# Kernel optimization log

Measured on AMD Instinct MI355X. Metric: run time of the kernel, lower is better.

## Reference

```python
import jax, jax.numpy as jnp
import numpy as np

B, H, N = 512, 128, 32      # batch, horizon, lidar sectors
D = 75                      # state dim (32 sectors + 32 diff + 11 non-lidar)
NON_AUG = 17                # 11 non-lidar + 6 aux stats
SM = 32                     # sector_model_dim
HALF = 128                  # embed_dim // 2
EMB = 256                   # embed_dim
DYAW_IDX = 72               # 64 + 3 + 2 + 2 + 1
NO_ECHO = 0.95


def linear(x, W, b):
    # torch nn.Linear: y = x @ W.T + b, W: (out, in)
    return jnp.einsum('...i,oi->...o', x, W) + b


def layernorm(x, w, b, eps=1e-5):
    m = x.mean(-1, keepdims=True)
    v = ((x - m) ** 2).mean(-1, keepdims=True)
    return (x - m) / jnp.sqrt(v + eps) * w + b


def setup_inputs() -> dict:
    key = jax.random.key(0)
    ks = jax.random.split(key, 10)
    f32 = jnp.float32
    return {
        'state_seq': jax.random.uniform(ks[0], (B, H, D), dtype=f32),
        'token_W': jax.random.normal(ks[1], (SM, 3), dtype=f32) * 0.3,
        'token_b': jnp.zeros((SM,), f32),
        'query_W': jax.random.normal(ks[2], (SM, NON_AUG), dtype=f32) * 0.2,
        'query_b': jnp.zeros((SM,), f32),
        'range_bias_scale': jnp.asarray(1.0, f32),
        'valid_bias': jnp.asarray(0.0, f32),
        'invalid_bias': jnp.asarray(-1.0, f32),
        'att_ln_w': jnp.ones((SM,), f32),
        'att_ln_b': jnp.zeros((SM,), f32),
        'non_W': jax.random.normal(ks[3], (HALF, NON_AUG), dtype=f32) * 0.2,
        'non_b': jnp.zeros((HALF,), f32),
        'spfb_W': jax.random.normal(ks[4], (HALF, 3), dtype=f32) * 0.3,
        'spfb_b': jnp.zeros((HALF,), f32),
        'sp_gate': jnp.asarray(-4.0, f32),
        'spatial_W': jax.random.normal(ks[5], (HALF, SM), dtype=f32) * 0.15,
        'spatial_b': jnp.zeros((HALF,), f32),
        'fuse_W': jax.random.normal(ks[6], (EMB, 2 * HALF), dtype=f32) * 0.06,
        'fuse_b': jnp.zeros((EMB,), f32),
        'ln_w': jnp.ones((EMB,), f32),
        'ln_b': jnp.zeros((EMB,), f32),
    }


def _forward(state_seq, token_W, token_b, query_W, query_b,
             range_bias_scale, valid_bias, invalid_bias, att_ln_w, att_ln_b,
             non_W, non_b, spfb_W, spfb_b, sp_gate,
             spatial_W, spatial_b, fuse_W, fuse_b, ln_w, ln_b):
    sectors = state_seq[:, :, 0:N]            # (B,H,N)
    lidar_diff = state_seq[:, :, N:2 * N]     # (B,H,N)
    non_lidar = state_seq[:, :, 2 * N:D]      # (B,H,11)

    valid = (sectors < NO_ECHO).astype(state_seq.dtype)
    min_r = sectors.min(axis=-1)
    mean_r = sectors.mean(axis=-1)
    valid_ratio = valid.mean(axis=-1)
    diff_abs = jnp.abs(lidar_diff)
    diff_abs_mean = diff_abs.mean(axis=-1)
    diff_abs_max = diff_abs.max(axis=-1)
    dyaw_abs = jnp.clip(jnp.abs(state_seq[:, :, DYAW_IDX]), 0.0, 1.0)
    diff_mag = jnp.clip(diff_abs_mean, 0.0, 1.0)

    aux = jnp.stack([min_r, mean_r, valid_ratio, diff_abs_mean, diff_abs_max, dyaw_abs], axis=-1)
    non_aug = jnp.concatenate([non_lidar, aux], axis=-1)  # (B,H,17)
    non_emb = jax.nn.relu(linear(non_aug, non_W, non_b))  # (B,H,HALF)

    sp_fallback = jnp.stack([min_r, mean_r, valid_ratio], axis=-1)
    sp_fallback_emb = jax.nn.relu(linear(sp_fallback, spfb_W, spfb_b))

    # --- spatial sector attention ---
    tok = jnp.stack([sectors, lidar_diff, valid], axis=-1)        # (B,H,N,3)
    tok_emb = jax.nn.relu(linear(tok, token_W, token_b))          # (B,H,N,SM)
    q = jax.nn.relu(linear(non_aug, query_W, query_b))[:, :, None, :]  # (B,H,1,SM)
    score = (tok_emb * q).sum(axis=-1) / np.sqrt(SM)              # (B,H,N)
    score = score + range_bias_scale * (1.0 - sectors)
    score = score + valid_bias * valid + invalid_bias * (1.0 - valid)
    w = jax.nn.softmax(score, axis=-1)
    ctx = (w[..., None] * tok_emb).sum(axis=2)                    # (B,H,SM)
    ctx = layernorm(ctx, att_ln_w, att_ln_b)

    sp_att_emb = jax.nn.relu(linear(ctx, spatial_W, spatial_b))
    alpha = jax.nn.sigmoid(sp_gate)
    sp_emb = alpha * sp_att_emb + (1.0 - alpha) * sp_fallback_emb

    x = jnp.concatenate([non_emb, sp_emb], axis=-1)
    x = jax.nn.relu(linear(x, fuse_W, fuse_b))
    x = layernorm(x, ln_w, ln_b)
    time_feats = jnp.stack([diff_mag, dyaw_abs], axis=-1)
    return x, time_feats


def reference(state_seq, token_W, token_b, query_W, query_b,
              range_bias_scale, valid_bias, invalid_bias, att_ln_w, att_ln_b,
              non_W, non_b, spfb_W, spfb_b, sp_gate,
              spatial_W, spatial_b, fuse_W, fuse_b, ln_w, ln_b):
    return _forward(state_seq, token_W, token_b, query_W, query_b,
                    range_bias_scale, valid_bias, invalid_bias, att_ln_w, att_ln_b,
                    non_W, non_b, spfb_W, spfb_b, sp_gate,
                    spatial_W, spatial_b, fuse_W, fuse_b, ln_w, ln_b)
```

## Files before the change

### kernel.cpp

```cpp
#include <hip/hip_runtime.h>

#define BH      65536
#define DSTATE  75
#define EMBD    256
#define NROWS   16
#define NTHREADS 512
#define NBLOCKS (BH / NROWS)

typedef _Float16 h2    __attribute__((ext_vector_type(2)));
typedef _Float16 f16x8 __attribute__((ext_vector_type(8)));
typedef float    f32x4 __attribute__((ext_vector_type(4)));

__device__ __forceinline__ h2 u2h(unsigned int u) {
    union { unsigned int u; h2 h; } c; c.u = u; return c.h;
}
__device__ __forceinline__ unsigned int h2u(h2 h) {
    union { h2 h; unsigned int u; } c; c.h = h; return c.u;
}
__device__ __forceinline__ unsigned int packh2(float a, float b) {
    union { h2 h; unsigned int u; } c;
    c.h = h2{(_Float16)a, (_Float16)b}; return c.u;
}
__device__ __forceinline__ h2 pkrtz(float a, float b) {
#if __has_builtin(__builtin_amdgcn_cvt_pkrtz)
    auto r = __builtin_amdgcn_cvt_pkrtz(a, b);
    return *reinterpret_cast<h2*>(&r);
#else
    return h2{(_Float16)a, (_Float16)b};
#endif
}
__device__ __forceinline__ float fdot2(h2 a, h2 b, float c) {
#if __has_builtin(__builtin_amdgcn_fdot2)
    return __builtin_amdgcn_fdot2(a, b, c, false);
#else
    return c + (float)a[0] * (float)b[0] + (float)a[1] * (float)b[1];
#endif
}
__device__ __forceinline__ h2 pkfma(h2 a, h2 b, h2 c) {
#if __has_builtin(__builtin_elementwise_fma)
    return __builtin_elementwise_fma(a, b, c);
#else
    return a * b + c;
#endif
}

template<int CTRL>
__device__ __forceinline__ float dppmv(float x) {
    return __builtin_bit_cast(float,
        __builtin_amdgcn_update_dpp(0, __builtin_bit_cast(int, x), CTRL, 0xF, 0xF, true));
}
template<int IMM>
__device__ __forceinline__ float swz(float x) {
    return __builtin_bit_cast(float,
        __builtin_amdgcn_ds_swizzle(__builtin_bit_cast(int, x), IMM));
}
#define ROR1 0x121
#define ROR2 0x122
#define ROR4 0x124
#define ROR8 0x128
#define QXOR1 0xB1
#define SWZ_XOR16 0x401F
#define SWZ_BC8   0x0100

__device__ __forceinline__ float sum32(float x) {
    x += dppmv<ROR1>(x); x += dppmv<ROR2>(x);
    x += dppmv<ROR4>(x); x += dppmv<ROR8>(x);
    return x + swz<SWZ_XOR16>(x);
}
__device__ __forceinline__ float sum16(float x) {
    x += dppmv<ROR1>(x); x += dppmv<ROR2>(x);
    x += dppmv<ROR4>(x); x += dppmv<ROR8>(x);
    return x;
}

__global__ __launch_bounds__(256) void prep_w_kernel(
    const float* __restrict__ fuse_W, const float* __restrict__ non_W,
    const float* __restrict__ spatial_W, const float* __restrict__ query_W,
    const float* __restrict__ token_W, const float* __restrict__ token_b,
    unsigned short* __restrict__ ws)
{
    int id = blockIdx.x * 256 + threadIdx.x;
    if (id < 8192) {
        int wl = id & 63, ct = (id >> 6) & 15, ks = id >> 10;
        int n = ct * 16 + (wl & 15);
        int k0 = ks * 32 + (wl >> 4) * 8;
        const float* src = fuse_W + n * 256 + k0;
        float4 a = *reinterpret_cast<const float4*>(src);
        float4 b = *reinterpret_cast<const float4*>(src + 4);
        uint4 o = make_uint4(packh2(a.x, a.y), packh2(a.z, a.w),
                             packh2(b.x, b.y), packh2(b.z, b.w));
        reinterpret_cast<uint4*>(ws)[id] = o;
    } else if (id < 8704) {
        int i = id - 8192;
        int wl = i & 63, ct = i >> 6;
        int n = ct * 16 + (wl & 15);
        int k0 = (wl >> 4) * 8;
        float v[8];
        #pragma unroll
        for (int j = 0; j < 8; ++j) {
            int k = k0 + j;
            v[j] = (k < 17) ? non_W[n * 17 + k] : 0.0f;
        }
        uint4 o = make_uint4(packh2(v[0], v[1]), packh2(v[2], v[3]),
                             packh2(v[4], v[5]), packh2(v[6], v[7]));
        reinterpret_cast<uint4*>(ws)[8192 + i] = o;
    } else if (id < 9216) {
        int i = id - 8704;
        int wl = i & 63, ct = i >> 6;
        int n = ct * 16 + (wl & 15);
        int k0 = (wl >> 4) * 8;
        const float* src = spatial_W + n * 32 + k0;
        float4 a = *reinterpret_cast<const float4*>(src);
        float4 b = *reinterpret_cast<const float4*>(src + 4);
        uint4 o = make_uint4(packh2(a.x, a.y), packh2(a.z, a.w),
                             packh2(b.x, b.y), packh2(b.z, b.w));
        reinterpret_cast<uint4*>(ws)[8704 + i] = o;
    } else if (id < 9728) {
        int i = id - 9216;
        int feat = i >> 4, j = i & 15;
        int k0 = 2 * j, k1 = 2 * j + 1;
        float a = (k0 < 17) ? query_W[feat * 17 + k0] : 0.0f;
        float b = (k1 < 17) ? query_W[feat * 17 + k1] : 0.0f;
        unsigned int* qWh = reinterpret_cast<unsigned int*>(ws + 73728);
        qWh[i] = packh2(a, b);
    } else if (id < 9856) {
        int i = id - 9728;
        int tbl = i >> 5, k = i & 31;
        float v = (tbl < 3) ? token_W[3 * k + tbl] : token_b[k];
        unsigned int* TWb = reinterpret_cast<unsigned int*>(ws + 73728) + 512;
        TWb[i] = packh2(v, v);
    } else if (id < 9920) {
        int i = id - 9856;
        int tbl = i >> 4, j = i & 15;
        int k0 = 2 * j, k1 = 2 * j + 1;
        float a = (tbl < 3) ? token_W[3 * k0 + tbl] : token_b[k0];
        float b = (tbl < 3) ? token_W[3 * k1 + tbl] : token_b[k1];
        unsigned int* TWp = reinterpret_cast<unsigned int*>(ws + 73728) + 640;
        TWp[i] = packh2(a, b);
    }
}

__global__ __launch_bounds__(512, 4) void att_state_enc_kernel(
    const float* __restrict__ state,
    const float* __restrict__ query_b,
    const float* __restrict__ rbs_p, const float* __restrict__ vb_p, const float* __restrict__ ivb_p,
    const float* __restrict__ att_ln_w, const float* __restrict__ att_ln_b,
    const float* __restrict__ non_b,
    const float* __restrict__ spfb_W, const float* __restrict__ spfb_b,
    const float* __restrict__ sp_gate_p,
    const float* __restrict__ spatial_b,
    const unsigned short* __restrict__ Wf, const unsigned short* __restrict__ Wn,
    const unsigned short* __restrict__ Ws,
    const unsigned int* __restrict__ qWh, const unsigned int* __restrict__ TWb,
    const unsigned int* __restrict__ TWp,
    const float* __restrict__ fuse_b,
    const float* __restrict__ ln_w, const float* __restrict__ ln_b,
    float* __restrict__ out_x, float* __restrict__ out_tf)
{
    __shared__ __align__(16) float4 s_fb4[NROWS];
    __shared__ __align__(16) _Float16 s_na_h[NROWS][40];
    __shared__ __align__(16) _Float16 s_ctx_h[NROWS][40];
    __shared__ __align__(16) unsigned int s_q2[NROWS][16];
    __shared__ __align__(16) uint4 s_p4[NROWS][16];
    __shared__ __align__(16) _Float16 s_x[NROWS][280];
    __shared__ __align__(16) float2 s_part[NROWS][8];
    __shared__ __align__(16) float2 s_mr[NROWS];
    __shared__ float  s_tf[NROWS * 2];

    const int t = threadIdx.x;
    const int g = t >> 5;
    const int l = t & 31;
    const long rowbase = (long)blockIdx.x * NROWS;

    const float rbs = rbs_p[0];
    const float vb  = vb_p[0];
    const float ivb = ivb_p[0];

    const float qb = query_b[l];
    const uint4* qwp = reinterpret_cast<const uint4*>(qWh + l * 16);
    const uint4 qw0 = qwp[0], qw1 = qwp[1], qw2 = qwp[2];
    const h2 zero2 = h2{(_Float16)0.0f, (_Float16)0.0f};

    {
        const int row = g;
        const long gb = (rowbase + row) * DSTATE;

        float sec = state[gb + l];
        float dif = state[gb + 32 + l];
        float nl  = (l < 11) ? state[gb + 64 + l] : 0.0f;
        float vld = (sec < 0.95f) ? 1.0f : 0.0f;
        float da  = fabsf(dif);
        float mn = sec, sm = sec, vs = vld, ds = da, dmx = da;
        {
            mn = fminf(mn, dppmv<ROR1>(mn)); sm += dppmv<ROR1>(sm); vs += dppmv<ROR1>(vs);
            ds += dppmv<ROR1>(ds); dmx = fmaxf(dmx, dppmv<ROR1>(dmx));
            mn = fminf(mn, dppmv<ROR2>(mn)); sm += dppmv<ROR2>(sm); vs += dppmv<ROR2>(vs);
            ds += dppmv<ROR2>(ds); dmx = fmaxf(dmx, dppmv<ROR2>(dmx));
            mn = fminf(mn, dppmv<ROR4>(mn)); sm += dppmv<ROR4>(sm); vs += dppmv<ROR4>(vs);
            ds += dppmv<ROR4>(ds); dmx = fmaxf(dmx, dppmv<ROR4>(dmx));
            mn = fminf(mn, dppmv<ROR8>(mn)); sm += dppmv<ROR8>(sm); vs += dppmv<ROR8>(vs);
            ds += dppmv<ROR8>(ds); dmx = fmaxf(dmx, dppmv<ROR8>(dmx));
            mn = fminf(mn, swz<SWZ_XOR16>(mn)); sm += swz<SWZ_XOR16>(sm);
            vs += swz<SWZ_XOR16>(vs); ds += swz<SWZ_XOR16>(ds);
            dmx = fmaxf(dmx, swz<SWZ_XOR16>(dmx));
        }
        const float min_r = mn, mean_r = sm * (1.0f/32.0f), vr = vs * (1.0f/32.0f);
        const float dam = ds * (1.0f/32.0f), dax = dmx;
        const float dyaw = fminf(fabsf(swz<SWZ_BC8>(nl)), 1.0f);

        float naval = 0.0f;
        if (l < 11)       naval = nl;
        else if (l == 11) naval = min_r;
        else if (l == 12) naval = mean_r;
        else if (l == 13) naval = vr;
        else if (l == 14) naval = dam;
        else if (l == 15) naval = dax;
        else if (l == 16) naval = dyaw;
        s_na_h[row][l] = (_Float16)naval;
        if (l == 0) {
            s_fb4[row] = make_float4(min_r, mean_r, vr, 0.0f);
            s_tf[row * 2] = fminf(dam, 1.0f); s_tf[row * 2 + 1] = dyaw;
        }

        {
            const uint4* nap = reinterpret_cast<const uint4*>(&s_na_h[row][0]);
            uint4 n0 = nap[0], n1 = nap[1], n2 = nap[2];
            float a0 = qb, a1 = 0.0f;
            a0 = fdot2(u2h(qw0.x), u2h(n0.x), a0);
            a1 = fdot2(u2h(qw0.y), u2h(n0.y), a1);
            a0 = fdot2(u2h(qw0.z), u2h(n0.z), a0);
            a1 = fdot2(u2h(qw0.w), u2h(n0.w), a1);
            a0 = fdot2(u2h(qw1.x), u2h(n1.x), a0);
            a1 = fdot2(u2h(qw1.y), u2h(n1.y), a1);
            a0 = fdot2(u2h(qw1.z), u2h(n1.z), a0);
            a1 = fdot2(u2h(qw1.w), u2h(n1.w), a1);
            a0 = fdot2(u2h(qw2.x), u2h(n2.x), a0);
            float qv = fmaxf(a0 + a1, 0.0f);
            float qn = dppmv<QXOR1>(qv);
            if ((l & 1) == 0) s_q2[row][l >> 1] = h2u(pkrtz(qv, qn));
        }

        {
            unsigned int q2[16];
            *reinterpret_cast<uint4*>(&q2[0])  = *reinterpret_cast<const uint4*>(&s_q2[row][0]);
            *reinterpret_cast<uint4*>(&q2[4])  = *reinterpret_cast<const uint4*>(&s_q2[row][4]);
            *reinterpret_cast<uint4*>(&q2[8])  = *reinterpret_cast<const uint4*>(&s_q2[row][8]);
            *reinterpret_cast<uint4*>(&q2[12]) = *reinterpret_cast<const uint4*>(&s_q2[row][12]);
            const h2 sec2 = pkrtz(sec, sec);
            const h2 dif2 = pkrtz(dif, dif);
            const h2 vld2 = pkrtz(vld, vld);
            float a0 = 0.0f, a1 = 0.0f;
            #pragma unroll
            for (int j = 0; j < 16; j += 2) {
                h2 z0 = pkfma(vld2, u2h(TWp[32 + j]), u2h(TWp[48 + j]));
                z0 = pkfma(dif2, u2h(TWp[16 + j]), z0);
                z0 = pkfma(sec2, u2h(TWp[j]), z0);
                z0 = __builtin_elementwise_max(z0, zero2);
                a0 = fdot2(z0, u2h(q2[j]), a0);
                h2 z1 = pkfma(vld2, u2h(TWp[33 + j]), u2h(TWp[49 + j]));
                z1 = pkfma(dif2, u2h(TWp[17 + j]), z1);
                z1 = pkfma(sec2, u2h(TWp[1 + j]), z1);
                z1 = __builtin_elementwise_max(z1, zero2);
                a1 = fdot2(z1, u2h(q2[j + 1]), a1);
            }
            float score = (a0 + a1) * 0.17677669529663687f
                        + rbs * (1.0f - sec) + vb * vld + ivb * (1.0f - vld);
            score = fminf(fmaxf(score, -60.0f), 60.0f);
            float e = __expf(score - 20.0f);
            float se = sum32(e);
            float w = __fdividef(e, se);
            float wn = dppmv<QXOR1>(w);
            float sn = dppmv<QXOR1>(sec);
            float dn = dppmv<QXOR1>(dif);
            float vn = dppmv<QXOR1>(vld);
            if ((l & 1) == 0) {
                uint4 pk = make_uint4(h2u(pkrtz(w, wn)), h2u(pkrtz(sec, sn)),
                                      h2u(pkrtz(dif, dn)), h2u(pkrtz(vld, vn)));
                s_p4[row][l >> 1] = pk;
            }
        }

        {
            const h2 tw0b = u2h(TWb[l]);
            const h2 tw1b = u2h(TWb[32 + l]);
            const h2 tw2b = u2h(TWb[64 + l]);
            const h2 tbb  = u2h(TWb[96 + l]);
            float a0 = 0.0f, a1 = 0.0f;
            #pragma unroll
            for (int i = 0; i < 16; i += 2) {
                uint4 p0 = s_p4[row][i];
                h2 z0 = pkfma(u2h(p0.w), tw2b, tbb);
                z0 = pkfma(u2h(p0.z), tw1b, z0);
                z0 = pkfma(u2h(p0.y), tw0b, z0);
                z0 = __builtin_elementwise_max(z0, zero2);
                a0 = fdot2(u2h(p0.x), z0, a0);
                uint4 p1 = s_p4[row][i + 1];
                h2 z1 = pkfma(u2h(p1.w), tw2b, tbb);
                z1 = pkfma(u2h(p1.z), tw1b, z1);
                z1 = pkfma(u2h(p1.y), tw0b, z1);
                z1 = __builtin_elementwise_max(z1, zero2);
                a1 = fdot2(u2h(p1.x), z1, a1);
            }
            float acc = a0 + a1;
            float smv = acc, sq = acc * acc;
            smv += dppmv<ROR1>(smv); sq += dppmv<ROR1>(sq);
            smv += dppmv<ROR2>(smv); sq += dppmv<ROR2>(sq);
            smv += dppmv<ROR4>(smv); sq += dppmv<ROR4>(sq);
            smv += dppmv<ROR8>(smv); sq += dppmv<ROR8>(sq);
            smv += swz<SWZ_XOR16>(smv); sq += swz<SWZ_XOR16>(sq);
            float mean = smv * (1.0f/32.0f);
            float var  = sq * (1.0f/32.0f) - mean * mean;
            float rstd = rsqrtf(var + 1e-5f);
            float ctx = (acc - mean) * rstd * att_ln_w[l] + att_ln_b[l];
            s_ctx_h[row][l] = (_Float16)ctx;
        }
    }
    __syncthreads();

    const int wid = t >> 6, wl = t & 63;
    const int arow = wl & 15, kg = wl >> 4;

    {
        if (t < NROWS * 2) out_tf[rowbase * 2 + t] = s_tf[t];

        const float alpha = 1.0f / (1.0f + __expf(-sp_gate_p[0]));
        float mnr[4], mer[4], vrr[4];
        #pragma unroll
        for (int r = 0; r < 4; ++r) {
            float4 fb4 = s_fb4[kg * 4 + r];
            mnr[r] = fb4.x; mer[r] = fb4.y; vrr[r] = fb4.z;
        }
        f16x8 a_na  = *reinterpret_cast<const f16x8*>(&s_na_h[arow][kg * 8]);
        f16x8 a_ctx = *reinterpret_cast<const f16x8*>(&s_ctx_h[arow][kg * 8]);

        const int ct = wid;
        const int col = ct * 16 + arow;
        f16x8 bN = *reinterpret_cast<const f16x8*>(Wn + ((ct * 64) + wl) * 8);
        f16x8 bS = *reinterpret_cast<const f16x8*>(Ws + ((ct * 64) + wl) * 8);
        f32x4 accN = __builtin_amdgcn_mfma_f32_16x16x32_f16(a_na,  bN, f32x4{0.f,0.f,0.f,0.f}, 0,0,0);
        f32x4 accS = __builtin_amdgcn_mfma_f32_16x16x32_f16(a_ctx, bS, f32x4{0.f,0.f,0.f,0.f}, 0,0,0);
        const float nb = non_b[col], sb = spatial_b[col];
        const float w0 = spfb_W[col*3], w1 = spfb_W[col*3+1], w2 = spfb_W[col*3+2];
        const float fbb = spfb_b[col];
        #pragma unroll
        for (int r = 0; r < 4; ++r) {
            const int row = kg * 4 + r;
            float ne = fmaxf(accN[r] + nb, 0.0f);
            float sa = fmaxf(accS[r] + sb, 0.0f);
            float fb = fmaxf(fbb + w0*mnr[r] + w1*mer[r] + w2*vrr[r], 0.0f);
            float sp = alpha * sa + (1.0f - alpha) * fb;
            float nen = dppmv<QXOR1>(ne);
            float spn = dppmv<QXOR1>(sp);
            if ((arow & 1) == 0) {
                *reinterpret_cast<unsigned int*>(&s_x[row][col])       = h2u(pkrtz(ne, nen));
                *reinterpret_cast<unsigned int*>(&s_x[row][128 + col]) = h2u(pkrtz(sp, spn));
            }
        }
    }
    __syncthreads();

    float v[2][4];
    {
        f32x4 acc[2];
        #pragma unroll
        for (int i = 0; i < 2; ++i) acc[i] = f32x4{0.f, 0.f, 0.f, 0.f};
        #pragma unroll
        for (int ks = 0; ks < 8; ++ks) {
            f16x8 a = *reinterpret_cast<const f16x8*>(&s_x[arow][ks * 32 + kg * 8]);
            #pragma unroll
            for (int i = 0; i < 2; ++i) {
                const int ct = wid * 2 + i;
                f16x8 b = *reinterpret_cast<const f16x8*>(Wf + (((ks * 16 + ct) * 64) + wl) * 8);
                acc[i] = __builtin_amdgcn_mfma_f32_16x16x32_f16(a, b, acc[i], 0, 0, 0);
            }
        }
        float psum[4] = {0.f, 0.f, 0.f, 0.f};
        float psq[4]  = {0.f, 0.f, 0.f, 0.f};
        #pragma unroll
        for (int i = 0; i < 2; ++i) {
            const int col = (wid * 2 + i) * 16 + arow;
            const float bias = fuse_b[col];
            #pragma unroll
            for (int r = 0; r < 4; ++r) {
                float x = fmaxf(acc[i][r] + bias, 0.0f);
                v[i][r] = x;
                psum[r] += x;
                psq[r]  += x * x;
            }
        }
        #pragma unroll
        for (int r = 0; r < 4; ++r) {
            psum[r] = sum16(psum[r]);
            psq[r]  = sum16(psq[r]);
        }
        if (arow == 0) {
            #pragma unroll
            for (int r = 0; r < 4; ++r)
                s_part[kg * 4 + r][wid] = make_float2(psum[r], psq[r]);
        }
    }
    __syncthreads();

    if (t < NROWS) {
        const float4* pp = reinterpret_cast<const float4*>(&s_part[t][0]);
        float4 pa = pp[0], pb = pp[1], pc = pp[2], pd = pp[3];
        float sum = pa.x + pa.z + pb.x + pb.z + pc.x + pc.z + pd.x + pd.z;
        float sq  = pa.y + pa.w + pb.y + pb.w + pc.y + pc.w + pd.y + pd.w;
        float mean = sum * (1.0f/256.0f);
        float var  = sq * (1.0f/256.0f) - mean * mean;
        float rstd = rsqrtf(var + 1e-5f);
        s_mr[t] = make_float2(mean, rstd);
    }
    __syncthreads();

    {
        float lwv[2], lbv[2];
        #pragma unroll
        for (int i = 0; i < 2; ++i) {
            const int col = (wid * 2 + i) * 16 + arow;
            lwv[i] = ln_w[col]; lbv[i] = ln_b[col];
        }
        #pragma unroll
        for (int r = 0; r < 4; ++r) {
            const int row = kg * 4 + r;
            float2 mr = s_mr[row];
            const long obase = (rowbase + row) * EMBD;
            #pragma unroll
            for (int i = 0; i < 2; ++i) {
                const int col = (wid * 2 + i) * 16 + arow;
                out_x[obase + col] = (v[i][r] - mr.x) * mr.y * lwv[i] + lbv[i];
            }
        }
    }
}

extern "C" void kernel_launch(void* const* d_in, const int* in_sizes, int n_in,
                              void* d_out, int out_size, void* d_ws, size_t ws_size,
                              hipStream_t stream) {
    const float* state     = (const float*)d_in[0];
    const float* token_W   = (const float*)d_in[1];
    const float* token_b   = (const float*)d_in[2];
    const float* query_W   = (const float*)d_in[3];
    const float* query_b   = (const float*)d_in[4];
    const float* rbs       = (const float*)d_in[5];
    const float* vbias     = (const float*)d_in[6];
    const float* ivbias    = (const float*)d_in[7];
    const float* att_ln_w  = (const float*)d_in[8];
    const float* att_ln_b  = (const float*)d_in[9];
    const float* non_W     = (const float*)d_in[10];
    const float* non_b     = (const float*)d_in[11];
    const float* spfb_W    = (const float*)d_in[12];
    const float* spfb_b    = (const float*)d_in[13];
    const float* sp_gate   = (const float*)d_in[14];
    const float* spatial_W = (const float*)d_in[15];
    const float* spatial_b = (const float*)d_in[16];
    const float* fuse_W    = (const float*)d_in[17];
    const float* fuse_b    = (const float*)d_in[18];
    const float* ln_w      = (const float*)d_in[19];
    const float* ln_b      = (const float*)d_in[20];

    float* out_x  = (float*)d_out;
    float* out_tf = out_x + (size_t)BH * EMBD;

    unsigned short* wsu = (unsigned short*)d_ws;
    const unsigned short* Wf = wsu;
    const unsigned short* Wn = wsu + 65536;
    const unsigned short* Ws = wsu + 65536 + 4096;
    const unsigned int* qWh = (const unsigned int*)(wsu + 73728);
    const unsigned int* TWb = qWh + 512;
    const unsigned int* TWp = TWb + 128;

    hipLaunchKernelGGL(prep_w_kernel, dim3(39), dim3(256), 0, stream,
                       fuse_W, non_W, spatial_W, query_W, token_W, token_b, wsu);

    hipLaunchKernelGGL(att_state_enc_kernel, dim3(NBLOCKS), dim3(NTHREADS), 0, stream,
        state, query_b, rbs, vbias, ivbias,
        att_ln_w, att_ln_b, non_b, spfb_W, spfb_b, sp_gate, spatial_b,
        Wf, Wn, Ws, qWh, TWb, TWp, fuse_b, ln_w, ln_b, out_x, out_tf);
}
```

Before: 57.00 us.

## Split fused encoder into front attention kernel and back MFMA kernel via workspace

Splits the single fused kernel into two. A front kernel handles the per-row stats, query, softmax attention and context layernorm with 8 rows per 256-thread block, and writes fp16 packed non-aug/ctx vectors plus fallback stats to workspace. A back kernel then does the MFMA projections, fuse GEMM and final layernorm on 32 rows per block, so each fuse-weight fetch is reused across more rows. The aim is to stop the two phases from limiting each other's occupancy and to improve weight reuse, at the cost of an extra launch and an intermediate global round-trip. The fused path stays as a fallback when the workspace is too small.

```diff
diff --git a/kernel.cpp b/kernel.cpp
--- a/kernel.cpp
+++ b/kernel.cpp
@@ -3,9 +3,6 @@
 #define BH      65536
 #define DSTATE  75
 #define EMBD    256
-#define NROWS   16
-#define NTHREADS 512
-#define NBLOCKS (BH / NROWS)
 
 typedef _Float16 h2    __attribute__((ext_vector_type(2)));
 typedef _Float16 f16x8 __attribute__((ext_vector_type(8)));
@@ -140,6 +137,312 @@
     }
 }
 
+__global__ __launch_bounds__(256, 8) void front_kernel(
+    const float* __restrict__ state,
+    const float* __restrict__ query_b,
+    const float* __restrict__ rbs_p, const float* __restrict__ vb_p, const float* __restrict__ ivb_p,
+    const float* __restrict__ att_ln_w, const float* __restrict__ att_ln_b,
+    const unsigned int* __restrict__ qWh, const unsigned int* __restrict__ TWb,
+    const unsigned int* __restrict__ TWp,
+    unsigned int* __restrict__ g_na, unsigned int* __restrict__ g_ctx,
+    float4* __restrict__ g_fb, float* __restrict__ out_tf)
+{
+    __shared__ __align__(16) _Float16 s_na_h[8][40];
+    __shared__ __align__(16) unsigned int s_q2[8][16];
+    __shared__ __align__(16) uint4 s_p4[8][16];
+
+    const int t = threadIdx.x;
+    const int g = t >> 5;
+    const int l = t & 31;
+    const long row = (long)blockIdx.x * 8 + g;
+    const long gb = row * DSTATE;
+
+    const float rbs = rbs_p[0];
+    const float vb  = vb_p[0];
+    const float ivb = ivb_p[0];
+    const float qb = query_b[l];
+    const uint4* qwp = reinterpret_cast<const uint4*>(qWh + l * 16);
+    const uint4 qw0 = qwp[0], qw1 = qwp[1], qw2 = qwp[2];
+    const h2 zero2 = h2{(_Float16)0.0f, (_Float16)0.0f};
+
+    float sec = state[gb + l];
+    float dif = state[gb + 32 + l];
+    float nl  = (l < 11) ? state[gb + 64 + l] : 0.0f;
+    float vld = (sec < 0.95f) ? 1.0f : 0.0f;
+    float da  = fabsf(dif);
+    float mn = sec, sm = sec, vs = vld, ds = da, dmx = da;
+    {
+        mn = fminf(mn, dppmv<ROR1>(mn)); sm += dppmv<ROR1>(sm); vs += dppmv<ROR1>(vs);
+        ds += dppmv<ROR1>(ds); dmx = fmaxf(dmx, dppmv<ROR1>(dmx));
+        mn = fminf(mn, dppmv<ROR2>(mn)); sm += dppmv<ROR2>(sm); vs += dppmv<ROR2>(vs);
+        ds += dppmv<ROR2>(ds); dmx = fmaxf(dmx, dppmv<ROR2>(dmx));
+        mn = fminf(mn, dppmv<ROR4>(mn)); sm += dppmv<ROR4>(sm); vs += dppmv<ROR4>(vs);
+        ds += dppmv<ROR4>(ds); dmx = fmaxf(dmx, dppmv<ROR4>(dmx));
+        mn = fminf(mn, dppmv<ROR8>(mn)); sm += dppmv<ROR8>(sm); vs += dppmv<ROR8>(vs);
+        ds += dppmv<ROR8>(ds); dmx = fmaxf(dmx, dppmv<ROR8>(dmx));
+        mn = fminf(mn, swz<SWZ_XOR16>(mn)); sm += swz<SWZ_XOR16>(sm);
+        vs += swz<SWZ_XOR16>(vs); ds += swz<SWZ_XOR16>(ds);
+        dmx = fmaxf(dmx, swz<SWZ_XOR16>(dmx));
+    }
+    const float min_r = mn, mean_r = sm * (1.0f/32.0f), vr = vs * (1.0f/32.0f);
+    const float dam = ds * (1.0f/32.0f), dax = dmx;
+    const float dyaw = fminf(fabsf(swz<SWZ_BC8>(nl)), 1.0f);
+
+    float naval = 0.0f;
+    if (l < 11)       naval = nl;
+    else if (l == 11) naval = min_r;
+    else if (l == 12) naval = mean_r;
+    else if (l == 13) naval = vr;
+    else if (l == 14) naval = dam;
+    else if (l == 15) naval = dax;
+    else if (l == 16) naval = dyaw;
+    s_na_h[g][l] = (_Float16)naval;
+    {
+        float nan_ = dppmv<QXOR1>(naval);
+        if ((l & 1) == 0) g_na[row * 16 + (l >> 1)] = h2u(pkrtz(naval, nan_));
+    }
+    if (l == 0) {
+        g_fb[row] = make_float4(min_r, mean_r, vr, 0.0f);
+        *reinterpret_cast<float2*>(out_tf + row * 2) =
+            make_float2(fminf(dam, 1.0f), dyaw);
+    }
+
+    {
+        const uint4* nap = reinterpret_cast<const uint4*>(&s_na_h[g][0]);
+        uint4 n0 = nap[0], n1 = nap[1], n2 = nap[2];
+        float a0 = qb, a1 = 0.0f;
+        a0 = fdot2(u2h(qw0.x), u2h(n0.x), a0);
+        a1 = fdot2(u2h(qw0.y), u2h(n0.y), a1);
+        a0 = fdot2(u2h(qw0.z), u2h(n0.z), a0);
+        a1 = fdot2(u2h(qw0.w), u2h(n0.w), a1);
+        a0 = fdot2(u2h(qw1.x), u2h(n1.x), a0);
+        a1 = fdot2(u2h(qw1.y), u2h(n1.y), a1);
+        a0 = fdot2(u2h(qw1.z), u2h(n1.z), a0);
+        a1 = fdot2(u2h(qw1.w), u2h(n1.w), a1);
+        a0 = fdot2(u2h(qw2.x), u2h(n2.x), a0);
+        float qv = fmaxf(a0 + a1, 0.0f);
+        float qn = dppmv<QXOR1>(qv);
+        if ((l & 1) == 0) s_q2[g][l >> 1] = h2u(pkrtz(qv, qn));
+    }
+
+    {
+        unsigned int q2[16];
+        *reinterpret_cast<uint4*>(&q2[0])  = *reinterpret_cast<const uint4*>(&s_q2[g][0]);
+        *reinterpret_cast<uint4*>(&q2[4])  = *reinterpret_cast<const uint4*>(&s_q2[g][4]);
+        *reinterpret_cast<uint4*>(&q2[8])  = *reinterpret_cast<const uint4*>(&s_q2[g][8]);
+        *reinterpret_cast<uint4*>(&q2[12]) = *reinterpret_cast<const uint4*>(&s_q2[g][12]);
+        const h2 sec2 = pkrtz(sec, sec);
+        const h2 dif2 = pkrtz(dif, dif);
+        const h2 vld2 = pkrtz(vld, vld);
+        float a0 = 0.0f, a1 = 0.0f;
+        #pragma unroll
+        for (int j = 0; j < 16; j += 2) {
+            h2 z0 = pkfma(vld2, u2h(TWp[32 + j]), u2h(TWp[48 + j]));
+            z0 = pkfma(dif2, u2h(TWp[16 + j]), z0);
+            z0 = pkfma(sec2, u2h(TWp[j]), z0);
+            z0 = __builtin_elementwise_max(z0, zero2);
+            a0 = fdot2(z0, u2h(q2[j]), a0);
+            h2 z1 = pkfma(vld2, u2h(TWp[33 + j]), u2h(TWp[49 + j]));
+            z1 = pkfma(dif2, u2h(TWp[17 + j]), z1);
+            z1 = pkfma(sec2, u2h(TWp[1 + j]), z1);
+            z1 = __builtin_elementwise_max(z1, zero2);
+            a1 = fdot2(z1, u2h(q2[j + 1]), a1);
+        }
+        float score = (a0 + a1) * 0.17677669529663687f
+                    + rbs * (1.0f - sec) + vb * vld + ivb * (1.0f - vld);
+        score = fminf(fmaxf(score, -60.0f), 60.0f);
+        float e = __expf(score - 20.0f);
+        float se = sum32(e);
+        float w = __fdividef(e, se);
+        float wn = dppmv<QXOR1>(w);
+        float sn = dppmv<QXOR1>(sec);
+        float dn = dppmv<QXOR1>(dif);
+        float vn = dppmv<QXOR1>(vld);
+        if ((l & 1) == 0) {
+            uint4 pk = make_uint4(h2u(pkrtz(w, wn)), h2u(pkrtz(sec, sn)),
+                                  h2u(pkrtz(dif, dn)), h2u(pkrtz(vld, vn)));
+            s_p4[g][l >> 1] = pk;
+        }
+    }
+
+    {
+        const h2 tw0b = u2h(TWb[l]);
+        const h2 tw1b = u2h(TWb[32 + l]);
+        const h2 tw2b = u2h(TWb[64 + l]);
+        const h2 tbb  = u2h(TWb[96 + l]);
+        float a0 = 0.0f, a1 = 0.0f;
+        #pragma unroll
+        for (int i = 0; i < 16; i += 2) {
+            uint4 p0 = s_p4[g][i];
+            h2 z0 = pkfma(u2h(p0.w), tw2b, tbb);
+            z0 = pkfma(u2h(p0.z), tw1b, z0);
+            z0 = pkfma(u2h(p0.y), tw0b, z0);
+            z0 = __builtin_elementwise_max(z0, zero2);
+            a0 = fdot2(u2h(p0.x), z0, a0);
+            uint4 p1 = s_p4[g][i + 1];
+            h2 z1 = pkfma(u2h(p1.w), tw2b, tbb);
+            z1 = pkfma(u2h(p1.z), tw1b, z1);
+            z1 = pkfma(u2h(p1.y), tw0b, z1);
+            z1 = __builtin_elementwise_max(z1, zero2);
+            a1 = fdot2(u2h(p1.x), z1, a1);
+        }
+        float acc = a0 + a1;
+        float smv = acc, sq = acc * acc;
+        smv += dppmv<ROR1>(smv); sq += dppmv<ROR1>(sq);
+        smv += dppmv<ROR2>(smv); sq += dppmv<ROR2>(sq);
+        smv += dppmv<ROR4>(smv); sq += dppmv<ROR4>(sq);
+        smv += dppmv<ROR8>(smv); sq += dppmv<ROR8>(sq);
+        smv += swz<SWZ_XOR16>(smv); sq += swz<SWZ_XOR16>(sq);
+        float mean = smv * (1.0f/32.0f);
+        float var  = sq * (1.0f/32.0f) - mean * mean;
+        float rstd = rsqrtf(var + 1e-5f);
+        float ctx = (acc - mean) * rstd * att_ln_w[l] + att_ln_b[l];
+        float cn = dppmv<QXOR1>(ctx);
+        if ((l & 1) == 0) g_ctx[row * 16 + (l >> 1)] = h2u(pkrtz(ctx, cn));
+    }
+}
+
+__global__ __launch_bounds__(512, 4) void back_kernel(
+    const float* __restrict__ non_b, const float* __restrict__ spfb_W,
+    const float* __restrict__ spfb_b, const float* __restrict__ sp_gate_p,
+    const float* __restrict__ spatial_b,
+    const unsigned short* __restrict__ Wf, const unsigned short* __restrict__ Wn,
+    const unsigned short* __restrict__ Ws,
+    const float* __restrict__ fuse_b,
+    const float* __restrict__ ln_w, const float* __restrict__ ln_b,
+    const unsigned int* __restrict__ g_na, const unsigned int* __restrict__ g_ctx,
+    const float4* __restrict__ g_fb,
+    float* __restrict__ out_x)
+{
+    __shared__ __align__(16) _Float16 s_x[32][280];
+    __shared__ __align__(16) float4 s_fb4[32];
+    __shared__ __align__(16) float2 s_part[32][4];
+    __shared__ __align__(16) float2 s_mr[32];
+
+    const int t = threadIdx.x;
+    const long rowbase = (long)blockIdx.x * 32;
+    const int wid = t >> 6, wl = t & 63;
+    const int arow = wl & 15, kg = wl >> 4;
+    const int m = wid & 1, cq = wid >> 1;
+
+    if (t < 32) s_fb4[t] = g_fb[rowbase + t];
+    __syncthreads();
+
+    {
+        const float alpha = 1.0f / (1.0f + __expf(-sp_gate_p[0]));
+        const long frow = rowbase + m * 16 + arow;
+        f16x8 a_na  = *reinterpret_cast<const f16x8*>(g_na  + frow * 16 + kg * 4);
+        f16x8 a_ctx = *reinterpret_cast<const f16x8*>(g_ctx + frow * 16 + kg * 4);
+        float mnr[4], mer[4], vrr[4];
+        #pragma unroll
+        for (int r = 0; r < 4; ++r) {
+            float4 fb4 = s_fb4[m * 16 + kg * 4 + r];
+            mnr[r] = fb4.x; mer[r] = fb4.y; vrr[r] = fb4.z;
+        }
+        #pragma unroll
+        for (int tt = 0; tt < 2; ++tt) {
+            const int ct = cq + tt * 4;
+            const int col = ct * 16 + arow;
+            f16x8 bN = *reinterpret_cast<const f16x8*>(Wn + ((ct * 64) + wl) * 8);
+            f16x8 bS = *reinterpret_cast<const f16x8*>(Ws + ((ct * 64) + wl) * 8);
+            f32x4 accN = __builtin_amdgcn_mfma_f32_16x16x32_f16(a_na,  bN, f32x4{0.f,0.f,0.f,0.f}, 0,0,0);
+            f32x4 accS = __builtin_amdgcn_mfma_f32_16x16x32_f16(a_ctx, bS, f32x4{0.f,0.f,0.f,0.f}, 0,0,0);
+            const float nb = non_b[col], sb = spatial_b[col];
+            const float w0 = spfb_W[col*3], w1 = spfb_W[col*3+1], w2 = spfb_W[col*3+2];
+            const float fbb = spfb_b[col];
+            #pragma unroll
+            for (int r = 0; r < 4; ++r) {
+                const int row = m * 16 + kg * 4 + r;
+                float ne = fmaxf(accN[r] + nb, 0.0f);
+                float sa = fmaxf(accS[r] + sb, 0.0f);
+                float fb = fmaxf(fbb + w0*mnr[r] + w1*mer[r] + w2*vrr[r], 0.0f);
+                float sp = alpha * sa + (1.0f - alpha) * fb;
+                float nen = dppmv<QXOR1>(ne);
+                float spn = dppmv<QXOR1>(sp);
+                if ((arow & 1) == 0) {
+                    *reinterpret_cast<unsigned int*>(&s_x[row][col])       = h2u(pkrtz(ne, nen));
+                    *reinterpret_cast<unsigned int*>(&s_x[row][128 + col]) = h2u(pkrtz(sp, spn));
+                }
+            }
+        }
+    }
+    __syncthreads();
+
+    float v[4][4];
+    {
+        f32x4 acc[4];
+        #pragma unroll
+        for (int i = 0; i < 4; ++i) acc[i] = f32x4{0.f, 0.f, 0.f, 0.f};
+        #pragma unroll
+        for (int ks = 0; ks < 8; ++ks) {
+            f16x8 a = *reinterpret_cast<const f16x8*>(&s_x[m * 16 + arow][ks * 32 + kg * 8]);
+            #pragma unroll
+            for (int i = 0; i < 4; ++i) {
+                const int ct = cq * 4 + i;
+                f16x8 b = *reinterpret_cast<const f16x8*>(Wf + (((ks * 16 + ct) * 64) + wl) * 8);
+                acc[i] = __builtin_amdgcn_mfma_f32_16x16x32_f16(a, b, acc[i], 0, 0, 0);
+            }
+        }
+        float psum[4] = {0.f, 0.f, 0.f, 0.f};
+        float psq[4]  = {0.f, 0.f, 0.f, 0.f};
+        #pragma unroll
+        for (int i = 0; i < 4; ++i) {
+            const int col = (cq * 4 + i) * 16 + arow;
+            const float bias = fuse_b[col];
+            #pragma unroll
+            for (int r = 0; r < 4; ++r) {
+                float x = fmaxf(acc[i][r] + bias, 0.0f);
+                v[i][r] = x;
+                psum[r] += x;
+                psq[r]  += x * x;
+            }
+        }
+        #pragma unroll
+        for (int r = 0; r < 4; ++r) {
+            psum[r] = sum16(psum[r]);
+            psq[r]  = sum16(psq[r]);
+        }
+        if (arow == 0) {
+            #pragma unroll
+            for (int r = 0; r < 4; ++r)
+                s_part[m * 16 + kg * 4 + r][cq] = make_float2(psum[r], psq[r]);
+        }
+    }
+    __syncthreads();
+
+    if (t < 32) {
+        const float4* pp = reinterpret_cast<const float4*>(&s_part[t][0]);
+        float4 pa = pp[0], pb = pp[1];
+        float sum = pa.x + pa.z + pb.x + pb.z;
+        float sq  = pa.y + pa.w + pb.y + pb.w;
+        float mean = sum * (1.0f/256.0f);
+        float var  = sq * (1.0f/256.0f) - mean * mean;
+        float rstd = rsqrtf(var + 1e-5f);
+        s_mr[t] = make_float2(mean, rstd);
+    }
+    __syncthreads();
+
+    {
+        float lwv[4], lbv[4];
+        #pragma unroll
+        for (int i = 0; i < 4; ++i) {
+            const int col = (cq * 4 + i) * 16 + arow;
+            lwv[i] = ln_w[col]; lbv[i] = ln_b[col];
+        }
+        #pragma unroll
+        for (int r = 0; r < 4; ++r) {
+            const int row = m * 16 + kg * 4 + r;
+            float2 mr = s_mr[row];
+            const long obase = (rowbase + row) * EMBD;
+            #pragma unroll
+            for (int i = 0; i < 4; ++i) {
+                const int col = (cq * 4 + i) * 16 + arow;
+                out_x[obase + col] = (v[i][r] - mr.x) * mr.y * lwv[i] + lbv[i];
+            }
+        }
+    }
+}
+
 __global__ __launch_bounds__(512, 4) void att_state_enc_kernel(
     const float* __restrict__ state,
     const float* __restrict__ query_b,
@@ -157,25 +460,24 @@
     const float* __restrict__ ln_w, const float* __restrict__ ln_b,
     float* __restrict__ out_x, float* __restrict__ out_tf)
 {
-    __shared__ __align__(16) float4 s_fb4[NROWS];
-    __shared__ __align__(16) _Float16 s_na_h[NROWS][40];
-    __shared__ __align__(16) _Float16 s_ctx_h[NROWS][40];
-    __shared__ __align__(16) unsigned int s_q2[NROWS][16];
-    __shared__ __align__(16) uint4 s_p4[NROWS][16];
-    __shared__ __align__(16) _Float16 s_x[NROWS][280];
-    __shared__ __align__(16) float2 s_part[NROWS][8];
-    __shared__ __align__(16) float2 s_mr[NROWS];
-    __shared__ float  s_tf[NROWS * 2];
+    __shared__ __align__(16) float4 s_fb4[16];
+    __shared__ __align__(16) _Float16 s_na_h[16][40];
+    __shared__ __align__(16) _Float16 s_ctx_h[16][40];
+    __shared__ __align__(16) unsigned int s_q2[16][16];
+    __shared__ __align__(16) uint4 s_p4[16][16];
+    __shared__ __align__(16) _Float16 s_x[16][280];
+    __shared__ __align__(16) float2 s_part[16][8];
+    __shared__ __align__(16) float2 s_mr[16];
+    __shared__ float  s_tf[16 * 2];
 
     const int t = threadIdx.x;
     const int g = t >> 5;
     const int l = t & 31;
-    const long rowbase = (long)blockIdx.x * NROWS;
+    const long rowbase = (long)blockIdx.x * 16;
 
     const float rbs = rbs_p[0];
     const float vb  = vb_p[0];
     const float ivb = ivb_p[0];
-
     const float qb = query_b[l];
     const uint4* qwp = reinterpret_cast<const uint4*>(qWh + l * 16);
     const uint4 qw0 = qwp[0], qw1 = qwp[1], qw2 = qwp[2];
@@ -184,7 +486,6 @@
     {
         const int row = g;
         const long gb = (rowbase + row) * DSTATE;
-
         float sec = state[gb + l];
         float dif = state[gb + 32 + l];
         float nl  = (l < 11) ? state[gb + 64 + l] : 0.0f;
@@ -221,7 +522,6 @@
             s_fb4[row] = make_float4(min_r, mean_r, vr, 0.0f);
             s_tf[row * 2] = fminf(dam, 1.0f); s_tf[row * 2 + 1] = dyaw;
         }
-
         {
             const uint4* nap = reinterpret_cast<const uint4*>(&s_na_h[row][0]);
             uint4 n0 = nap[0], n1 = nap[1], n2 = nap[2];
@@ -239,7 +539,6 @@
             float qn = dppmv<QXOR1>(qv);
             if ((l & 1) == 0) s_q2[row][l >> 1] = h2u(pkrtz(qv, qn));
         }
-
         {
             unsigned int q2[16];
             *reinterpret_cast<uint4*>(&q2[0])  = *reinterpret_cast<const uint4*>(&s_q2[row][0]);
@@ -279,7 +578,6 @@
                 s_p4[row][l >> 1] = pk;
             }
         }
-
         {
             const h2 tw0b = u2h(TWb[l]);
             const h2 tw1b = u2h(TWb[32 + l]);
@@ -321,8 +619,7 @@
     const int arow = wl & 15, kg = wl >> 4;
 
     {
-        if (t < NROWS * 2) out_tf[rowbase * 2 + t] = s_tf[t];
-
+        if (t < 16 * 2) out_tf[rowbase * 2 + t] = s_tf[t];
         const float alpha = 1.0f / (1.0f + __expf(-sp_gate_p[0]));
         float mnr[4], mer[4], vrr[4];
         #pragma unroll
@@ -332,7 +629,6 @@
         }
         f16x8 a_na  = *reinterpret_cast<const f16x8*>(&s_na_h[arow][kg * 8]);
         f16x8 a_ctx = *reinterpret_cast<const f16x8*>(&s_ctx_h[arow][kg * 8]);
-
         const int ct = wid;
         const int col = ct * 16 + arow;
         f16x8 bN = *reinterpret_cast<const f16x8*>(Wn + ((ct * 64) + wl) * 8);
@@ -401,7 +697,7 @@
     }
     __syncthreads();
 
-    if (t < NROWS) {
+    if (t < 16) {
         const float4* pp = reinterpret_cast<const float4*>(&s_part[t][0]);
         float4 pa = pp[0], pb = pp[1], pc = pp[2], pd = pp[3];
         float sum = pa.x + pa.z + pb.x + pb.z + pc.x + pc.z + pd.x + pd.z;
@@ -473,8 +769,25 @@
     hipLaunchKernelGGL(prep_w_kernel, dim3(39), dim3(256), 0, stream,
                        fuse_W, non_W, spatial_W, query_W, token_W, token_b, wsu);
 
-    hipLaunchKernelGGL(att_state_enc_kernel, dim3(NBLOCKS), dim3(NTHREADS), 0, stream,
-        state, query_b, rbs, vbias, ivbias,
-        att_ln_w, att_ln_b, non_b, spfb_W, spfb_b, sp_gate, spatial_b,
-        Wf, Wn, Ws, qWh, TWb, TWp, fuse_b, ln_w, ln_b, out_x, out_tf);
-}
+    const size_t INTER_OFF = 151552;
+    const size_t NEED = INTER_OFF + (size_t)BH * 64 * 2 + (size_t)BH * 16;
+    if (ws_size >= NEED) {
+        unsigned int* g_na  = (unsigned int*)((char*)d_ws + INTER_OFF);
+        unsigned int* g_ctx = g_na + (size_t)BH * 16;
+        float4* g_fb = (float4*)(g_ctx + (size_t)BH * 16);
+
+        hipLaunchKernelGGL(front_kernel, dim3(BH / 8), dim3(256), 0, stream,
+            state, query_b, rbs, vbias, ivbias, att_ln_w, att_ln_b,
+            qWh, TWb, TWp, g_na, g_ctx, g_fb, out_tf);
+
+        hipLaunchKernelGGL(back_kernel, dim3(BH / 32), dim3(512), 0, stream,
+            non_b, spfb_W, spfb_b, sp_gate, spatial_b,
+            Wf, Wn, Ws, fuse_b, ln_w, ln_b,
+            g_na, g_ctx, g_fb, out_x);
+    } else {
+        hipLaunchKernelGGL(att_state_enc_kernel, dim3(BH / 16), dim3(512), 0, stream,
+            state, query_b, rbs, vbias, ivbias,
+            att_ln_w, att_ln_b, non_b, spfb_W, spfb_b, sp_gate, spatial_b,
+            Wf, Wn, Ws, qWh, TWb, TWp, fuse_b, ln_w, ln_b, out_x, out_tf);
+    }
+}
```

New measurement: 62.31 us. 9.3% more time.

## Process 32 rows per block with 2x4 warp tiling over MFMA tiles

Applied to the files above, without the earlier changes.

Doubles the rows handled per block from 16 to 32. Each wave in the first stage now processes two rows in an unrolled loop. The MFMA GEMM stages are re-tiled so each of the 8 waves owns one 16-row half and a quarter of the columns, which doubles reuse of each loaded weight fragment and halves the grid size. The cost is more registers per thread (4 accumulators, more values kept live), more shared memory, and fewer blocks to fill the GPU.

```diff
diff --git a/kernel.cpp b/kernel.cpp
--- a/kernel.cpp
+++ b/kernel.cpp
@@ -3,7 +3,7 @@
 #define BH      65536
 #define DSTATE  75
 #define EMBD    256
-#define NROWS   16
+#define NROWS   32
 #define NTHREADS 512
 #define NBLOCKS (BH / NROWS)
 
@@ -163,7 +163,7 @@
     __shared__ __align__(16) unsigned int s_q2[NROWS][16];
     __shared__ __align__(16) uint4 s_p4[NROWS][16];
     __shared__ __align__(16) _Float16 s_x[NROWS][280];
-    __shared__ __align__(16) float2 s_part[NROWS][8];
+    __shared__ __align__(16) float2 s_part[NROWS][4];
     __shared__ __align__(16) float2 s_mr[NROWS];
     __shared__ float  s_tf[NROWS * 2];
 
@@ -175,14 +175,14 @@
     const float rbs = rbs_p[0];
     const float vb  = vb_p[0];
     const float ivb = ivb_p[0];
-
     const float qb = query_b[l];
     const uint4* qwp = reinterpret_cast<const uint4*>(qWh + l * 16);
     const uint4 qw0 = qwp[0], qw1 = qwp[1], qw2 = qwp[2];
     const h2 zero2 = h2{(_Float16)0.0f, (_Float16)0.0f};
 
-    {
-        const int row = g;
+    #pragma unroll
+    for (int rr = 0; rr < 2; ++rr) {
+        const int row = g + 16 * rr;
         const long gb = (rowbase + row) * DSTATE;
 
         float sec = state[gb + l];
@@ -319,57 +319,61 @@
 
     const int wid = t >> 6, wl = t & 63;
     const int arow = wl & 15, kg = wl >> 4;
+    const int m = wid & 1, cq = wid >> 1;
 
     {
         if (t < NROWS * 2) out_tf[rowbase * 2 + t] = s_tf[t];
 
         const float alpha = 1.0f / (1.0f + __expf(-sp_gate_p[0]));
+        const int rbase = m * 16;
+        f16x8 a_na  = *reinterpret_cast<const f16x8*>(&s_na_h[rbase + arow][kg * 8]);
+        f16x8 a_ctx = *reinterpret_cast<const f16x8*>(&s_ctx_h[rbase + arow][kg * 8]);
         float mnr[4], mer[4], vrr[4];
         #pragma unroll
         for (int r = 0; r < 4; ++r) {
-            float4 fb4 = s_fb4[kg * 4 + r];
+            float4 fb4 = s_fb4[rbase + kg * 4 + r];
             mnr[r] = fb4.x; mer[r] = fb4.y; vrr[r] = fb4.z;
         }
-        f16x8 a_na  = *reinterpret_cast<const f16x8*>(&s_na_h[arow][kg * 8]);
-        f16x8 a_ctx = *reinterpret_cast<const f16x8*>(&s_ctx_h[arow][kg * 8]);
-
-        const int ct = wid;
-        const int col = ct * 16 + arow;
-        f16x8 bN = *reinterpret_cast<const f16x8*>(Wn + ((ct * 64) + wl) * 8);
-        f16x8 bS = *reinterpret_cast<const f16x8*>(Ws + ((ct * 64) + wl) * 8);
-        f32x4 accN = __builtin_amdgcn_mfma_f32_16x16x32_f16(a_na,  bN, f32x4{0.f,0.f,0.f,0.f}, 0,0,0);
-        f32x4 accS = __builtin_amdgcn_mfma_f32_16x16x32_f16(a_ctx, bS, f32x4{0.f,0.f,0.f,0.f}, 0,0,0);
-        const float nb = non_b[col], sb = spatial_b[col];
-        const float w0 = spfb_W[col*3], w1 = spfb_W[col*3+1], w2 = spfb_W[col*3+2];
-        const float fbb = spfb_b[col];
-        #pragma unroll
-        for (int r = 0; r < 4; ++r) {
-            const int row = kg * 4 + r;
-            float ne = fmaxf(accN[r] + nb, 0.0f);
-            float sa = fmaxf(accS[r] + sb, 0.0f);
-            float fb = fmaxf(fbb + w0*mnr[r] + w1*mer[r] + w2*vrr[r], 0.0f);
-            float sp = alpha * sa + (1.0f - alpha) * fb;
-            float nen = dppmv<QXOR1>(ne);
-            float spn = dppmv<QXOR1>(sp);
-            if ((arow & 1) == 0) {
-                *reinterpret_cast<unsigned int*>(&s_x[row][col])       = h2u(pkrtz(ne, nen));
-                *reinterpret_cast<unsigned int*>(&s_x[row][128 + col]) = h2u(pkrtz(sp, spn));
+        #pragma unroll
+        for (int tt = 0; tt < 2; ++tt) {
+            const int ct = cq + tt * 4;
+            const int col = ct * 16 + arow;
+            f16x8 bN = *reinterpret_cast<const f16x8*>(Wn + ((ct * 64) + wl) * 8);
+            f16x8 bS = *reinterpret_cast<const f16x8*>(Ws + ((ct * 64) + wl) * 8);
+            f32x4 accN = __builtin_amdgcn_mfma_f32_16x16x32_f16(a_na,  bN, f32x4{0.f,0.f,0.f,0.f}, 0,0,0);
+            f32x4 accS = __builtin_amdgcn_mfma_f32_16x16x32_f16(a_ctx, bS, f32x4{0.f,0.f,0.f,0.f}, 0,0,0);
+            const float nb = non_b[col], sb = spatial_b[col];
+            const float w0 = spfb_W[col*3], w1 = spfb_W[col*3+1], w2 = spfb_W[col*3+2];
+            const float fbb = spfb_b[col];
+            #pragma unroll
+            for (int r = 0; r < 4; ++r) {
+                const int row = rbase + kg * 4 + r;
+                float ne = fmaxf(accN[r] + nb, 0.0f);
+                float sa = fmaxf(accS[r] + sb, 0.0f);
+                float fb = fmaxf(fbb + w0*mnr[r] + w1*mer[r] + w2*vrr[r], 0.0f);
+                float sp = alpha * sa + (1.0f - alpha) * fb;
+                float nen = dppmv<QXOR1>(ne);
+                float spn = dppmv<QXOR1>(sp);
+                if ((arow & 1) == 0) {
+                    *reinterpret_cast<unsigned int*>(&s_x[row][col])       = h2u(pkrtz(ne, nen));
+                    *reinterpret_cast<unsigned int*>(&s_x[row][128 + col]) = h2u(pkrtz(sp, spn));
+                }
             }
         }
     }
     __syncthreads();
 
-    float v[2][4];
+    float v[4][4];
     {
-        f32x4 acc[2];
-        #pragma unroll
-        for (int i = 0; i < 2; ++i) acc[i] = f32x4{0.f, 0.f, 0.f, 0.f};
+        f32x4 acc[4];
+        #pragma unroll
+        for (int i = 0; i < 4; ++i) acc[i] = f32x4{0.f, 0.f, 0.f, 0.f};
         #pragma unroll
         for (int ks = 0; ks < 8; ++ks) {
-            f16x8 a = *reinterpret_cast<const f16x8*>(&s_x[arow][ks * 32 + kg * 8]);
-            #pragma unroll
-            for (int i = 0; i < 2; ++i) {
-                const int ct = wid * 2 + i;
+            f16x8 a = *reinterpret_cast<const f16x8*>(&s_x[m * 16 + arow][ks * 32 + kg * 8]);
+            #pragma unroll
+            for (int i = 0; i < 4; ++i) {
+                const int ct = cq * 4 + i;
                 f16x8 b = *reinterpret_cast<const f16x8*>(Wf + (((ks * 16 + ct) * 64) + wl) * 8);
                 acc[i] = __builtin_amdgcn_mfma_f32_16x16x32_f16(a, b, acc[i], 0, 0, 0);
             }
@@ -377,8 +381,8 @@
         float psum[4] = {0.f, 0.f, 0.f, 0.f};
         float psq[4]  = {0.f, 0.f, 0.f, 0.f};
         #pragma unroll
-        for (int i = 0; i < 2; ++i) {
-            const int col = (wid * 2 + i) * 16 + arow;
+        for (int i = 0; i < 4; ++i) {
+            const int col = (cq * 4 + i) * 16 + arow;
             const float bias = fuse_b[col];
             #pragma unroll
             for (int r = 0; r < 4; ++r) {
@@ -396,16 +400,16 @@
         if (arow == 0) {
             #pragma unroll
             for (int r = 0; r < 4; ++r)
-                s_part[kg * 4 + r][wid] = make_float2(psum[r], psq[r]);
+                s_part[m * 16 + kg * 4 + r][cq] = make_float2(psum[r], psq[r]);
         }
     }
     __syncthreads();
 
     if (t < NROWS) {
         const float4* pp = reinterpret_cast<const float4*>(&s_part[t][0]);
-        float4 pa = pp[0], pb = pp[1], pc = pp[2], pd = pp[3];
-        float sum = pa.x + pa.z + pb.x + pb.z + pc.x + pc.z + pd.x + pd.z;
-        float sq  = pa.y + pa.w + pb.y + pb.w + pc.y + pc.w + pd.y + pd.w;
+        float4 pa = pp[0], pb = pp[1];
+        float sum = pa.x + pa.z + pb.x + pb.z;
+        float sq  = pa.y + pa.w + pb.y + pb.w;
         float mean = sum * (1.0f/256.0f);
         float var  = sq * (1.0f/256.0f) - mean * mean;
         float rstd = rsqrtf(var + 1e-5f);
@@ -414,20 +418,20 @@
     __syncthreads();
 
     {
-        float lwv[2], lbv[2];
-        #pragma unroll
-        for (int i = 0; i < 2; ++i) {
-            const int col = (wid * 2 + i) * 16 + arow;
+        float lwv[4], lbv[4];
+        #pragma unroll
+        for (int i = 0; i < 4; ++i) {
+            const int col = (cq * 4 + i) * 16 + arow;
             lwv[i] = ln_w[col]; lbv[i] = ln_b[col];
         }
         #pragma unroll
         for (int r = 0; r < 4; ++r) {
-            const int row = kg * 4 + r;
+            const int row = m * 16 + kg * 4 + r;
             float2 mr = s_mr[row];
             const long obase = (rowbase + row) * EMBD;
             #pragma unroll
-            for (int i = 0; i < 2; ++i) {
-                const int col = (wid * 2 + i) * 16 + arow;
+            for (int i = 0; i < 4; ++i) {
+                const int col = (cq * 4 + i) * 16 + arow;
                 out_x[obase + col] = (v[i][r] - mr.x) * mr.y * lwv[i] + lbv[i];
             }
         }
```

Result: faster. 53.42 us (-6.3%).
